# Performance work log

Measured on AMD Instinct MI355X. Metric: run time of the kernel, lower is better.

The kernel has to match this reference:

```python
import jax, jax.numpy as jnp
import numpy as np

PATCHES = [(4, 4), (2, 2)]  # (width, height) per stream chunk
SCALE = 2
DM = 256


def conv2d(x, w, bias, pad=0):
    y = jax.lax.conv_general_dilated(
        x, w, window_strides=(1, 1), padding=[(pad, pad), (pad, pad)],
        dimension_numbers=("NCHW", "OIHW", "NCHW"))
    return y + bias[None, :, None, None]


def to_patches(x, b, t, dk, out_h, ph, out_w, pw):
    # x: [b*t, dk, out_h*ph, out_w*pw] -> [b, t*out_h*out_w, dk*ph*pw]
    x = x.reshape(b, t, dk, out_h, ph, out_w, pw)
    return x.transpose(0, 1, 3, 5, 2, 4, 6).reshape(b, t * out_h * out_w, dk * ph * pw)


def from_patches(y, b, t, dk, out_h, ph, out_w, pw):
    # y: [b, t*out_h*out_w, dk*ph*pw] -> [b*t, dk, out_h*ph, out_w*pw]
    y = y.reshape(b, t, out_h, out_w, dk, ph, pw)
    return y.transpose(0, 1, 4, 2, 5, 3, 6).reshape(b * t, dk, out_h * ph, out_w * pw)


def attention(q, k, v):
    d = q.shape[-1]
    scores = jnp.einsum("bnd,bmd->bnm", q, k) / jnp.sqrt(jnp.asarray(d, q.dtype))
    p = jax.nn.softmax(scores, axis=-1)
    return jnp.einsum("bnm,bmd->bnd", p, v)


def forward(x_lo, x_hi, b,
            wq_lo, bq_lo, wk_lo, bk_lo, wv_lo, bv_lo,
            wq_hi, bq_hi, wk_hi, bk_hi, wv_hi, bv_hi,
            wo_lo, bo_lo, wo_hi, bo_hi):
    bt_lo, _, h, w = x_lo.shape
    bt_hi, _, h_, w_ = x_hi.shape
    t_lo = bt_lo // b
    t_hi = bt_hi // b
    n_p = len(PATCHES)
    d_k_lo = DM * SCALE ** 2 // n_p
    d_k_hi = DM // n_p

    q_lo_all = conv2d(x_lo, wq_lo, bq_lo)
    k_lo_all = conv2d(x_lo, wk_lo, bk_lo)
    v_lo_all = conv2d(x_lo, wv_lo, bv_lo)
    q_hi_all = conv2d(x_hi, wq_hi, bq_hi)
    k_hi_all = conv2d(x_hi, wk_hi, bk_hi)
    v_hi_all = conv2d(x_hi, wv_hi, bv_hi)

    outs_lo, outs_hi = [], []
    for i, (width, height) in enumerate(PATCHES):
        out_w, out_h = w // width, h // height
        sl_lo = slice(i * d_k_lo, (i + 1) * d_k_lo)
        sl_hi = slice(i * d_k_hi, (i + 1) * d_k_hi)
        ql = to_patches(q_lo_all[:, sl_lo], b, t_lo, d_k_lo, out_h, height, out_w, width)
        kl = to_patches(k_lo_all[:, sl_lo], b, t_lo, d_k_lo, out_h, height, out_w, width)
        vl = to_patches(v_lo_all[:, sl_lo], b, t_lo, d_k_lo, out_h, height, out_w, width)
        qh = to_patches(q_hi_all[:, sl_hi], b, t_hi, d_k_hi, out_h, height * SCALE, out_w, width * SCALE)
        kh = to_patches(k_hi_all[:, sl_hi], b, t_hi, d_k_hi, out_h, height * SCALE, out_w, width * SCALE)
        vh = to_patches(v_hi_all[:, sl_hi], b, t_hi, d_k_hi, out_h, height * SCALE, out_w, width * SCALE)

        q = jnp.concatenate([ql, qh], axis=1)
        k = jnp.concatenate([kl, kh], axis=1)
        v = jnp.concatenate([vl, vh], axis=1)
        y = attention(q, k, v)

        n_lo = t_lo * out_h * out_w
        y_lo = from_patches(y[:, :n_lo], b, t_lo, d_k_lo, out_h, height, out_w, width)
        y_hi = from_patches(y[:, n_lo:], b, t_hi, d_k_hi, out_h, height * SCALE, out_w, width * SCALE)
        outs_lo.append(y_lo)
        outs_hi.append(y_hi)

    out_lo = jnp.concatenate(outs_lo, axis=1)
    out_hi = jnp.concatenate(outs_hi, axis=1)
    out_lo = jax.nn.leaky_relu(conv2d(out_lo, wo_lo, bo_lo, pad=1), 0.2)
    out_hi = jax.nn.leaky_relu(conv2d(out_hi, wo_hi, bo_hi, pad=1), 0.2)
    return out_lo, out_hi


def setup_inputs() -> dict:
    key = jax.random.key(0)
    ks = jax.random.split(key, 12)
    dm2 = DM * SCALE ** 2  # 1024
    s = 0.02
    inp = {
        "x_lo": jax.random.normal(ks[0], (16, DM, 32, 32), jnp.float32),
        "x_hi": jax.random.normal(ks[1], (16, DM, 64, 64), jnp.float32),
        "b": 4,
        "wq_lo": jax.random.normal(ks[2], (dm2, DM, 1, 1), jnp.float32) * s,
        "bq_lo": jnp.zeros((dm2,), jnp.float32),
        "wk_lo": jax.random.normal(ks[3], (dm2, DM, 1, 1), jnp.float32) * s,
        "bk_lo": jnp.zeros((dm2,), jnp.float32),
        "wv_lo": jax.random.normal(ks[4], (dm2, DM, 1, 1), jnp.float32) * s,
        "bv_lo": jnp.zeros((dm2,), jnp.float32),
        "wq_hi": jax.random.normal(ks[5], (DM, DM, 1, 1), jnp.float32) * s,
        "bq_hi": jnp.zeros((DM,), jnp.float32),
        "wk_hi": jax.random.normal(ks[6], (DM, DM, 1, 1), jnp.float32) * s,
        "bk_hi": jnp.zeros((DM,), jnp.float32),
        "wv_hi": jax.random.normal(ks[7], (DM, DM, 1, 1), jnp.float32) * s,
        "bv_hi": jnp.zeros((DM,), jnp.float32),
        "wo_lo": jax.random.normal(ks[8], (DM, dm2, 3, 3), jnp.float32) * s,
        "bo_lo": jnp.zeros((DM,), jnp.float32),
        "wo_hi": jax.random.normal(ks[9], (DM, DM, 3, 3), jnp.float32) * s,
        "bo_hi": jnp.zeros((DM,), jnp.float32),
    }
    return inp


def reference(x_lo, x_hi, b,
              wq_lo, bq_lo, wk_lo, bk_lo, wv_lo, bv_lo,
              wq_hi, bq_hi, wk_hi, bk_hi, wv_hi, bv_hi,
              wo_lo, bo_lo, wo_hi, bo_hi):
    return forward(x_lo, x_hi, b,
                   wq_lo, bq_lo, wk_lo, bk_lo, wv_lo, bv_lo,
                   wq_hi, bq_hi, wk_hi, bk_hi, wv_hi, bv_hi,
                   wo_lo, bo_lo, wo_hi, bo_hi)
```

## Files before the change

kernel.cpp:

```cpp
#include <hip/hip_runtime.h>
#include <hip/hip_bf16.h>
#include <stdint.h>

typedef __attribute__((ext_vector_type(8))) short short8;
typedef __attribute__((ext_vector_type(4))) short short4v;
typedef __attribute__((ext_vector_type(2))) short short2v;
typedef __attribute__((ext_vector_type(4))) float floatx4;

__device__ __forceinline__ unsigned short f2b(float f) {
  unsigned u = __builtin_bit_cast(unsigned, f);
  unsigned r = u + 0x7fffu + ((u >> 16) & 1u);
  return (unsigned short)(r >> 16);
}
__device__ __forceinline__ float b2f(unsigned short h) {
  unsigned u = ((unsigned)h) << 16;
  return __builtin_bit_cast(float, u);
}
__device__ __forceinline__ void glds16(const unsigned short* src, unsigned short* dst) {
  __builtin_amdgcn_global_load_lds((const __attribute__((address_space(1))) void*)src,
                                   (__attribute__((address_space(3))) void*)dst, 16, 0, 0);
}
__device__ __forceinline__ int swz(int r, int o) {
  return (r << 9) + (o ^ ((((o >> 7) & 3) ^ (r & 7)) << 4));
}
__device__ __forceinline__ void xcd_remap(int& bx, int& by, int& bz) {
  const int gx = gridDim.x, gy = gridDim.y;
  const int nwg = gx * gy * (int)gridDim.z;
  int lin = bx + gx * (by + gy * bz);
  lin = (lin & 7) * (nwg >> 3) + (lin >> 3);
  bx = lin % gx; const int r = lin / gx;
  by = r % gy; bz = r / gy;
}

struct GemmP {
  const unsigned short* A;
  const unsigned short* B;
  long sAb, sBb;
  int lda, ldb, K;
  unsigned short* C; long sCb; int ldc;
  const float* bias;
  unsigned short *Q0, *K0, *V0t, *Q1, *K1, *V1t;
};

template<int EPI>
__global__ __launch_bounds__(512) void gemm256(GemmP p) {
  __shared__ __align__(16) unsigned short LDS[65536];
  const int tid = threadIdx.x;
  const int wv = tid >> 6, lane = tid & 63;
  const int wm = wv >> 2, wn = wv & 3;
  const int g = lane >> 4, l16 = lane & 15;
  int bx = blockIdx.x, by = blockIdx.y, bz = blockIdx.z;
  xcd_remap(bx, by, bz);
  const int m0 = by * 256, n0 = bx * 256;

  int bb = bz, koff = 0, Keff = p.K;
  if constexpr (EPI == 1) { bb = bz >> 4; koff = (bz & 15) * (p.K >> 4); Keff = p.K >> 4; }
  const unsigned short* Ab = p.A + (long)bb * p.sAb + (long)m0 * p.lda + koff;
  const unsigned short* Bb = p.B + (long)bb * p.sBb + (long)n0 * p.ldb + koff;
  const int NT = Keff >> 5;

  const int r0 = tid >> 2;
  const int cs = (tid & 3) ^ ((r0 >> 1) & 3);
  const unsigned short* aS0 = Ab + (long)r0 * p.lda + cs * 8;
  const unsigned short* aS1 = aS0 + (long)128 * p.lda;
  const unsigned short* bS0 = Bb + (long)r0 * p.ldb + cs * 8;
  const unsigned short* bS1 = bS0 + (long)128 * p.ldb;
  unsigned short* const lds0 = (unsigned short*)LDS;
  const int wbase = wv * 512;

  auto STAGE_A = [&](int t) {
    unsigned short* d = lds0 + (t & 3) * 16384;
    const long ko = (long)t * 32;
    glds16(aS0 + ko, d + wbase);
    glds16(aS1 + ko, d + 4096 + wbase);
  };
  auto STAGE_B = [&](int t) {
    unsigned short* d = lds0 + (t & 3) * 16384 + 8192;
    const long ko = (long)t * 32;
    glds16(bS0 + ko, d + wbase);
    glds16(bS1 + ko, d + 4096 + wbase);
  };

  STAGE_A(0); STAGE_B(0); STAGE_A(1); STAGE_B(1); STAGE_A(2); STAGE_B(2);

  floatx4 acc[8][4];
  const floatx4 z4 = {0.f, 0.f, 0.f, 0.f};
#pragma unroll
  for (int i = 0; i < 8; ++i)
#pragma unroll
    for (int j = 0; j < 4; ++j) acc[i][j] = z4;

  const int loff = l16 * 32 + ((g ^ ((l16 >> 1) & 3)) * 8);
  const int aRowB = wm * 128;

  asm volatile("s_waitcnt vmcnt(8)" ::: "memory");
  __builtin_amdgcn_s_barrier();
  short8 bf[4], af[4];
#pragma unroll
  for (int ni = 0; ni < 4; ++ni)
    bf[ni] = *(const short8*)(lds0 + 8192 + (wn * 64 + ni * 16) * 32 + loff);
#pragma unroll
  for (int mi = 0; mi < 4; ++mi)
    af[mi] = *(const short8*)(lds0 + (aRowB + mi * 16) * 32 + loff);

  for (int t = 0; t < NT; ++t) {
    const unsigned short* As = lds0 + (t & 3) * 16384;
    const unsigned short* AsN = lds0 + ((t + 1) & 3) * 16384;
    if (t < NT - 2) asm volatile("s_waitcnt vmcnt(4)" ::: "memory");
    else            asm volatile("s_waitcnt vmcnt(0)" ::: "memory");
    __builtin_amdgcn_s_barrier();
    __builtin_amdgcn_sched_barrier(0);
    if (t + 3 < NT) STAGE_A(t + 3);
    short8 ag[4];
#pragma unroll
    for (int mi = 0; mi < 4; ++mi)
      ag[mi] = *(const short8*)(As + (aRowB + 64 + mi * 16) * 32 + loff);
    __builtin_amdgcn_s_setprio(1);
#pragma unroll
    for (int mi = 0; mi < 4; ++mi)
#pragma unroll
      for (int ni = 0; ni < 4; ++ni)
        acc[mi][ni] = __builtin_amdgcn_mfma_f32_16x16x32_bf16(af[mi], bf[ni], acc[mi][ni], 0, 0, 0);
    __builtin_amdgcn_s_setprio(0);
    if (t + 3 < NT) STAGE_B(t + 3);
    short8 bfN[4], afN[4];
    if (t + 1 < NT) {
      const unsigned short* BsN = AsN + 8192;
#pragma unroll
      for (int ni = 0; ni < 4; ++ni)
        bfN[ni] = *(const short8*)(BsN + (wn * 64 + ni * 16) * 32 + loff);
#pragma unroll
      for (int mi = 0; mi < 4; ++mi)
        afN[mi] = *(const short8*)(AsN + (aRowB + mi * 16) * 32 + loff);
    }
    __builtin_amdgcn_s_setprio(1);
#pragma unroll
    for (int mi = 0; mi < 4; ++mi)
#pragma unroll
      for (int ni = 0; ni < 4; ++ni)
        acc[4 + mi][ni] = __builtin_amdgcn_mfma_f32_16x16x32_bf16(ag[mi], bf[ni], acc[4 + mi][ni], 0, 0, 0);
    __builtin_amdgcn_s_setprio(0);
    if (t + 1 < NT) {
#pragma unroll
      for (int i = 0; i < 4; ++i) { bf[i] = bfN[i]; af[i] = afN[i]; }
    }
  }

  if constexpr (EPI == 1) {
    unsigned short* C = p.C + (long)bz * p.sCb;
#pragma unroll
    for (int mi = 0; mi < 8; ++mi) {
#pragma unroll
      for (int ni = 0; ni < 4; ++ni) {
        const int col = n0 + wn * 64 + ni * 16 + l16;
#pragma unroll
        for (int r4 = 0; r4 < 4; ++r4) {
          const int row = m0 + wm * 128 + mi * 16 + g * 4 + r4;
          C[(long)row * p.ldc + col] = f2b(acc[mi][ni][r4]);
        }
      }
    }
  } else {
    __syncthreads();
    char* shb = (char*)LDS;
    const int sel = (EPI == 2) ? (m0 >> 10) : (m0 >> 8);
#pragma unroll
    for (int mi = 0; mi < 8; ++mi) {
#pragma unroll
      for (int ni = 0; ni < 4; ++ni) {
        const int c = wn * 64 + ni * 16 + l16;
#pragma unroll
        for (int r4 = 0; r4 < 4; ++r4) {
          const int rr = wm * 128 + mi * 16 + g * 4 + r4;
          float v = acc[mi][ni][r4];
          if constexpr (EPI == 2 || EPI == 3) {
            v += p.bias[m0 + rr];
            if (sel == 0) {
              float sc;
              if constexpr (EPI == 2) sc = ((m0 & 1023) < 512) ? 0.011048543456039806f
                                                               : 0.02209708691207961f;
              else                    sc = (rr < 128) ? 0.011048543456039806f
                                                      : 0.02209708691207961f;
              v *= sc;
            }
          }
          *(unsigned short*)(shb + swz(rr, c * 2)) = f2b(v);
        }
      }
    }
    __syncthreads();

    if constexpr (EPI == 0) {
      unsigned short* C = p.C + (long)bz * p.sCb;
#pragma unroll
      for (int j = 0; j < 16; ++j) {
        const int e = j * 512 + tid;
        const int r = e >> 5, ck = e & 31;
        short8 v = *(const short8*)(shb + swz(r, ck * 16));
        *(short8*)(C + (long)(m0 + r) * p.ldc + n0 + ck * 8) = v;
      }
    } else if constexpr (EPI == 2) {
      const int chb = m0 & 1023;
      const bool cfg0 = chb < 512;
      const int b = bz >> 2, tt = bz & 3;
      const int k0 = n0 >> 8;
      unsigned short* dst = cfg0 ? (sel == 0 ? p.Q0 : sel == 1 ? p.K0 : p.V0t)
                                 : (sel == 0 ? p.Q1 : sel == 1 ? p.K1 : p.V1t);
      if (sel != 2) {
        if (cfg0) {
          const long base = (long)(b * 512) * 8192;
#pragma unroll
          for (int j = 0; j < 16; ++j) {
            const int e = j * 512 + tid;
            const int pi = e >> 9, idx2 = e & 511;
            const int ch = idx2 >> 1, hf = idx2 & 1;
            const int oyL = pi >> 3, ox = pi & 7;
            const int nseq = (tt * 8 + 2 * k0 + oyL) * 8 + ox;
            const int yl = oyL * 4 + hf * 2;
            short4v a = *(const short4v*)(shb + swz(ch, (yl * 32 + ox * 4) * 2));
            short4v b2 = *(const short4v*)(shb + swz(ch, ((yl + 1) * 32 + ox * 4) * 2));
            short8 v = {a[0], a[1], a[2], a[3], b2[0], b2[1], b2[2], b2[3]};
            *(short8*)(dst + base + (long)nseq * 8192 + (chb + ch) * 16 + hf * 8) = v;
          }
        } else {
          const int c2lo = chb - 512;
          const long base = (long)(b * 2048) * 2048;
#pragma unroll
          for (int j = 0; j < 16; ++j) {
            const int e = j * 512 + tid;
            const int pi = e >> 7, cp = e & 127;
            const int oyL = pi >> 4, ox = pi & 15;
            const int nseq = (tt * 16 + 4 * k0 + oyL) * 16 + ox;
            short8 v;
#pragma unroll
            for (int rr = 0; rr < 2; ++rr) {
#pragma unroll
              for (int k = 0; k < 2; ++k) {
                short2v pr = *(const short2v*)(shb +
                    swz(cp * 2 + rr, ((oyL * 2 + k) * 32 + ox * 2) * 2));
                v[rr * 4 + k * 2] = pr[0];
                v[rr * 4 + k * 2 + 1] = pr[1];
              }
            }
            *(short8*)(dst + base + (long)nseq * 2048 + (c2lo + cp * 2) * 4) = v;
          }
        }
      } else {
        if (cfg0) {
          const long base = (long)(b * 8192) * 512;
#pragma unroll
          for (int j = 0; j < 16; ++j) {
            const int e = j * 512 + tid;
            const int oyL = e >> 12, fu = e & 4095;
            const int ch = fu >> 4, pp = fu & 15;
            const int py = pp >> 2, px = pp & 3;
            const int yl = oyL * 4 + py;
            short8 v;
#pragma unroll
            for (int ox = 0; ox < 8; ++ox)
              v[ox] = *(const unsigned short*)(shb + swz(ch, (yl * 32 + ox * 4 + px) * 2));
            const long f = (long)(chb + ch) * 16 + pp;
            *(short8*)(dst + base + f * 512 + (tt * 8 + 2 * k0 + oyL) * 8) = v;
          }
        } else {
          const int c2lo = chb - 512;
          const long base = (long)(b * 2048) * 2048;
#pragma unroll
          for (int j = 0; j < 16; ++j) {
            const int e = j * 512 + tid;
            const int he = e & 1, oyL = (e >> 1) & 3, fu = e >> 3;
            const int c2 = fu >> 2, pp = fu & 3;
            const int py = pp >> 1, px = pp & 1;
            const int yl = oyL * 2 + py;
            short8 v;
#pragma unroll
            for (int i = 0; i < 8; ++i) {
              const int ox = he * 8 + i;
              v[i] = *(const unsigned short*)(shb + swz(c2, (yl * 32 + ox * 2 + px) * 2));
            }
            const long f = (long)(c2lo + c2) * 4 + pp;
            *(short8*)(dst + base + f * 2048 + (tt * 16 + 4 * k0 + oyL) * 16 + he * 8) = v;
          }
        }
      }
    } else if constexpr (EPI == 3) {
      const int b = bz >> 2, tt = bz & 3;
      const int k0 = n0 >> 8;
      const int oyA = k0 >> 1, pyb = (k0 & 1) * 4;
      unsigned short* dstA = sel == 0 ? p.Q0 : sel == 1 ? p.K0 : p.V0t;
      unsigned short* dstB = sel == 0 ? p.Q1 : sel == 1 ? p.K1 : p.V1t;
      if (sel != 2) {
#pragma unroll
        for (int j = 0; j < 16; ++j) {
          const int e = j * 512 + tid;
          if (e < 4096) {
            const int ox = e >> 9, cy = e & 511;
            const int ch = cy >> 2, yl = cy & 3;
            const int nseq = 256 + (tt * 8 + oyA) * 8 + ox;
            short8 v = *(const short8*)(shb + swz(ch, (yl * 64 + ox * 8) * 2));
            *(short8*)(dstA + ((long)(b * 512 + nseq)) * 8192 + ch * 64 + (pyb + yl) * 8) = v;
          } else {
            const int ee = e - 4096;
            const int ox = ee >> 8, cc = ee & 255;
            const int c2 = cc >> 1, hf = cc & 1;
            const int nseq = 1024 + (tt * 16 + k0) * 16 + ox;
            short8 v;
#pragma unroll
            for (int k = 0; k < 2; ++k) {
              short4v a = *(const short4v*)(shb +
                  swz(128 + c2, ((hf * 2 + k) * 64 + ox * 4) * 2));
              v[k * 4] = a[0]; v[k * 4 + 1] = a[1]; v[k * 4 + 2] = a[2]; v[k * 4 + 3] = a[3];
            }
            *(short8*)(dstB + ((long)(b * 2048 + nseq)) * 2048 + c2 * 16 + hf * 8) = v;
          }
        }
      } else {
#pragma unroll
        for (int j = 0; j < 16; ++j) {
          const int e = j * 512 + tid;
          if (e < 4096) {
            const int ch = e >> 5, yl = (e >> 3) & 3, px = e & 7;
            short8 v;
#pragma unroll
            for (int ox = 0; ox < 8; ++ox)
              v[ox] = *(const unsigned short*)(shb + swz(ch, (yl * 64 + ox * 8 + px) * 2));
            const long f = (long)ch * 64 + (pyb + yl) * 8 + px;
            *(short8*)(dstA + ((long)b * 8192 + f) * 512 + 256 + (tt * 8 + oyA) * 8) = v;
          } else {
            const int ee = e - 4096;
            const int he = ee & 1, fu = ee >> 1;
            const int c2 = fu >> 4, pp = fu & 15;
            const int py = pp >> 2, px = pp & 3;
            short8 v;
#pragma unroll
            for (int i = 0; i < 8; ++i) {
              const int x = (he * 8 + i) * 4 + px;
              v[i] = *(const unsigned short*)(shb + swz(128 + c2, (py * 64 + x) * 2));
            }
            const long f = (long)c2 * 16 + pp;
            *(short8*)(dstB + ((long)b * 2048 + f) * 2048 + 1024 + (tt * 16 + k0) * 16 + he * 8) = v;
          }
        }
      }
    } else if constexpr (EPI == 4) {
      const int b = bz;
      if (m0 == 0) {
        const int chbase = n0 >> 4;
        unsigned short* dst = p.Q0;
#pragma unroll
        for (int j = 0; j < 16; ++j) {
          const int e = j * 512 + tid;
          const int hf = e & 1, pp = (e >> 1) & 15, rr = e >> 5;
          const int t = rr >> 6, oh = (rr >> 3) & 7, ow = rr & 7;
          const int bt = b * 4 + t;
          const int py = pp >> 2, px = pp & 3;
          short8 v;
#pragma unroll
          for (int i = 0; i < 8; ++i)
            v[i] = *(const unsigned short*)(shb + swz(rr, ((hf * 8 + i) * 16 + pp) * 2));
          *(short8*)(dst + (((long)bt * 34 + oh * 4 + py + 1) * 34 + ow * 4 + px + 1) * 1024
                     + chbase + hf * 8) = v;
        }
      } else {
        const int chbase = n0 >> 6;
        unsigned short* dst = p.Q1;
#pragma unroll
        for (int j = 0; j < 32; ++j) {
          const int e = j * 512 + tid;
          const int pp = e & 63, rr = e >> 6;
          const int t = rr >> 6, oh = (rr >> 3) & 7, ow = rr & 7;
          const int bt = b * 4 + t;
          const int py = pp >> 3, px = pp & 7;
          short4v v;
#pragma unroll
          for (int i = 0; i < 4; ++i)
            v[i] = *(const unsigned short*)(shb + swz(rr, (i * 64 + pp) * 2));
          *(short4v*)(dst + (((long)bt * 66 + oh * 8 + py + 1) * 66 + ow * 8 + px + 1) * 256
                      + chbase) = v;
        }
      }
    } else if constexpr (EPI == 5) {
      const int b = bz;
      if (m0 < 1024) {
        const int chbase = n0 >> 2;
        unsigned short* dst = p.Q0;
#pragma unroll
        for (int j = 0; j < 16; ++j) {
          const int e = j * 512 + tid;
          const int ch8 = e & 7, pp = (e >> 3) & 3, rr = e >> 5;
          const int n = m0 + rr;
          const int t = n >> 8, oh = (n >> 4) & 15, ow = n & 15;
          const int bt = b * 4 + t;
          const int py = pp >> 1, px = pp & 1;
          short8 v;
#pragma unroll
          for (int i = 0; i < 8; ++i)
            v[i] = *(const unsigned short*)(shb + swz(rr, ((ch8 * 8 + i) * 4 + pp) * 2));
          *(short8*)(dst + (((long)bt * 34 + oh * 2 + py + 1) * 34 + ow * 2 + px + 1) * 1024
                     + 512 + chbase + ch8 * 8) = v;
        }
      } else {
        const int chbase = n0 >> 4;
        unsigned short* dst = p.Q1;
#pragma unroll
        for (int j = 0; j < 16; ++j) {
          const int e = j * 512 + tid;
          const int hf = e & 1, pp = (e >> 1) & 15, rr = e >> 5;
          const int m = m0 + rr - 1024;
          const int t = m >> 8, oh = (m >> 4) & 15, ow = m & 15;
          const int bt = b * 4 + t;
          const int py = pp >> 2, px = pp & 3;
          short8 v;
#pragma unroll
          for (int i = 0; i < 8; ++i)
            v[i] = *(const unsigned short*)(shb + swz(rr, ((hf * 8 + i) * 16 + pp) * 2));
          *(short8*)(dst + (((long)bt * 66 + oh * 4 + py + 1) * 66 + ow * 4 + px + 1) * 256
                     + 128 + chbase + hf * 8) = v;
        }
      }
    }
  }
}

template<int H, int W, int CIN, int KS, bool PARTIAL>
__global__ __launch_bounds__(512) void conv256(const unsigned short* __restrict__ Cinp,
                                               const unsigned short* __restrict__ Wt,
                                               const float* __restrict__ bias,
                                               float* __restrict__ out,
                                               unsigned short* __restrict__ P0,
                                               unsigned short* __restrict__ P1) {
  constexpr int HP = H + 2, WP = W + 2;
  constexpr int CC = CIN / KS;
  constexpr int NT = 9 * CC / 32;
  __shared__ __align__(16) unsigned short LDS[65536];
  const int tid = threadIdx.x;
  const int wv = tid >> 6, lane = tid & 63;
  const int wm = wv >> 2, wn = wv & 3;
  const int g = lane >> 4, l16 = lane & 15;
  int bx = blockIdx.x, by = blockIdx.y, bz = blockIdx.z;
  xcd_remap(bx, by, bz);
  const int bt = bz / KS, ks = bz % KS;
  const int n0 = bx * 256;

  const int r0 = tid >> 2;
  const int cs = (tid & 3) ^ ((r0 >> 1) & 3);
  const unsigned short* wA0 = Wt + (long)r0 * CIN + ks * CC + cs * 8;
  const unsigned short* wA1 = wA0 + (long)128 * CIN;
  const int p0 = n0 + r0, p1 = p0 + 128;
  const int y0p = p0 / W, x0p = p0 % W;
  const int y1p = p1 / W, x1p = p1 % W;
  const unsigned short* cB = Cinp + (long)bt * HP * WP * CIN + ks * CC + cs * 8;
  const unsigned short* pB0 = cB + ((long)y0p * WP + x0p) * CIN;
  const unsigned short* pB1 = cB + ((long)y1p * WP + x1p) * CIN;
  unsigned short* const lds0 = (unsigned short*)LDS;
  const int wbase = wv * 512;

  auto STAGE_A = [&](int t) {
    unsigned short* d = lds0 + (t & 3) * 16384;
    const int tap = t >> 3, tc = (t & 7) * 32;
    const long off = (long)tap * (256L * CIN) + tc;
    glds16(wA0 + off, d + wbase);
    glds16(wA1 + off, d + 4096 + wbase);
  };
  auto STAGE_B = [&](int t) {
    unsigned short* d = lds0 + (t & 3) * 16384 + 8192;
    const int tap = t >> 3, tc = (t & 7) * 32;
    const int ky = tap / 3, kx = tap - ky * 3;
    const long off = ((long)ky * WP + kx) * CIN + tc;
    glds16(pB0 + off, d + wbase);
    glds16(pB1 + off, d + 4096 + wbase);
  };

  STAGE_A(0); STAGE_B(0); STAGE_A(1); STAGE_B(1); STAGE_A(2); STAGE_B(2);

  floatx4 acc[8][4];
  const floatx4 z4 = {0.f, 0.f, 0.f, 0.f};
#pragma unroll
  for (int i = 0; i < 8; ++i)
#pragma unroll
    for (int j = 0; j < 4; ++j) acc[i][j] = z4;

  const int loff = l16 * 32 + ((g ^ ((l16 >> 1) & 3)) * 8);
  const int aRowB = wm * 128;

  asm volatile("s_waitcnt vmcnt(8)" ::: "memory");
  __builtin_amdgcn_s_barrier();
  short8 bf[4], af[4];
#pragma unroll
  for (int ni = 0; ni < 4; ++ni)
    bf[ni] = *(const short8*)(lds0 + 8192 + (wn * 64 + ni * 16) * 32 + loff);
#pragma unroll
  for (int mi = 0; mi < 4; ++mi)
    af[mi] = *(const short8*)(lds0 + (aRowB + mi * 16) * 32 + loff);

  for (int t = 0; t < NT; ++t) {
    const unsigned short* As = lds0 + (t & 3) * 16384;
    const unsigned short* AsN = lds0 + ((t + 1) & 3) * 16384;
    if (t < NT - 2) asm volatile("s_waitcnt vmcnt(4)" ::: "memory");
    else            asm volatile("s_waitcnt vmcnt(0)" ::: "memory");
    __builtin_amdgcn_s_barrier();
    __builtin_amdgcn_sched_barrier(0);
    if (t + 3 < NT) STAGE_A(t + 3);
    short8 ag[4];
#pragma unroll
    for (int mi = 0; mi < 4; ++mi)
      ag[mi] = *(const short8*)(As + (aRowB + 64 + mi * 16) * 32 + loff);
    __builtin_amdgcn_s_setprio(1);
#pragma unroll
    for (int mi = 0; mi < 4; ++mi)
#pragma unroll
      for (int ni = 0; ni < 4; ++ni)
        acc[mi][ni] = __builtin_amdgcn_mfma_f32_16x16x32_bf16(af[mi], bf[ni], acc[mi][ni], 0, 0, 0);
    __builtin_amdgcn_s_setprio(0);
    if (t + 3 < NT) STAGE_B(t + 3);
    short8 bfN[4], afN[4];
    if (t + 1 < NT) {
      const unsigned short* BsN = AsN + 8192;
#pragma unroll
      for (int ni = 0; ni < 4; ++ni)
        bfN[ni] = *(const short8*)(BsN + (wn * 64 + ni * 16) * 32 + loff);
#pragma unroll
      for (int mi = 0; mi < 4; ++mi)
        afN[mi] = *(const short8*)(AsN + (aRowB + mi * 16) * 32 + loff);
    }
    __builtin_amdgcn_s_setprio(1);
#pragma unroll
    for (int mi = 0; mi < 4; ++mi)
#pragma unroll
      for (int ni = 0; ni < 4; ++ni)
        acc[4 + mi][ni] = __builtin_amdgcn_mfma_f32_16x16x32_bf16(ag[mi], bf[ni], acc[4 + mi][ni], 0, 0, 0);
    __builtin_amdgcn_s_setprio(0);
    if (t + 1 < NT) {
#pragma unroll
      for (int i = 0; i < 4; ++i) { bf[i] = bfN[i]; af[i] = afN[i]; }
    }
  }

  if constexpr (!PARTIAL) {
#pragma unroll
    for (int mi = 0; mi < 8; ++mi) {
#pragma unroll
      for (int ni = 0; ni < 4; ++ni) {
        const int pn = n0 + wn * 64 + ni * 16 + l16;
        const int y = pn / W, x = pn % W;
#pragma unroll
        for (int r4 = 0; r4 < 4; ++r4) {
          const int co = wm * 128 + mi * 16 + g * 4 + r4;
          float v = acc[mi][ni][r4] + bias[co];
          v = v > 0.f ? v : 0.2f * v;
          out[(((long)bt * 256 + co) * H + y) * W + x] = v;
        }
      }
    }
  } else {
    unsigned short* pout = (ks < 2 ? P0 : P1) + (long)(ks & 1) * (16L * 256 * H * W);
#pragma unroll
    for (int mi = 0; mi < 8; ++mi) {
#pragma unroll
      for (int ni = 0; ni < 4; ++ni) {
        const int pn = n0 + wn * 64 + ni * 16 + l16;
        const int y = pn / W, x = pn % W;
#pragma unroll
        for (int r4 = 0; r4 < 4; ++r4) {
          const int co = wm * 128 + mi * 16 + g * 4 + r4;
          pout[(((long)bt * 256 + co) * H + y) * W + x] = f2b(acc[mi][ni][r4]);
        }
      }
    }
  }
}

template<int L>
__global__ __launch_bounds__(256) void softmax_rows(unsigned short* S) {
  const int w = threadIdx.x >> 6, lane = threadIdx.x & 63;
  const long row = (long)blockIdx.x * 4 + w;
  unsigned short* R = S + row * L;
  constexpr int NC = L / 64;
  float v[NC];
  float m = -1e30f;
#pragma unroll
  for (int i = 0; i < NC; ++i) { v[i] = b2f(R[i * 64 + lane]); m = fmaxf(m, v[i]); }
#pragma unroll
  for (int off = 32; off; off >>= 1) m = fmaxf(m, __shfl_xor(m, off, 64));
  float s = 0.f;
#pragma unroll
  for (int i = 0; i < NC; ++i) { v[i] = __expf(v[i] - m); s += v[i]; }
#pragma unroll
  for (int off = 32; off; off >>= 1) s += __shfl_xor(s, off, 64);
  const float inv = 1.0f / s;
#pragma unroll
  for (int i = 0; i < NC; ++i) R[i * 64 + lane] = f2b(v[i] * inv);
}

__global__ __launch_bounds__(256) void softmax_red16(const unsigned short* __restrict__ P,
                                                     unsigned short* __restrict__ S) {
  const int w = threadIdx.x >> 6, lane = threadIdx.x & 63;
  const int rowg = blockIdx.x * 4 + w;
  const int b = rowg >> 9, n = rowg & 511;
  const unsigned short* base = P + ((long)b * 16) * 262144 + (long)n * 512 + lane;
  float v[8];
#pragma unroll
  for (int i = 0; i < 8; ++i) {
    float s = 0.f;
#pragma unroll
    for (int ks = 0; ks < 16; ++ks) s += b2f(base[(long)ks * 262144 + i * 64]);
    v[i] = s;
  }
  float m = -1e30f;
#pragma unroll
  for (int i = 0; i < 8; ++i) m = fmaxf(m, v[i]);
#pragma unroll
  for (int off = 32; off; off >>= 1) m = fmaxf(m, __shfl_xor(m, off, 64));
  float s = 0.f;
#pragma unroll
  for (int i = 0; i < 8; ++i) { v[i] = __expf(v[i] - m); s += v[i]; }
#pragma unroll
  for (int off = 32; off; off >>= 1) s += __shfl_xor(s, off, 64);
  const float inv = 1.0f / s;
  unsigned short* R = S + (long)rowg * 512;
#pragma unroll
  for (int i = 0; i < 8; ++i) R[i * 64 + lane] = f2b(v[i] * inv);
}

__global__ __launch_bounds__(256) void xt_both(const float* __restrict__ x_lo,
                                               unsigned short* __restrict__ xt_lo,
                                               const float* __restrict__ x_hi,
                                               unsigned short* __restrict__ xt_hi) {
  __shared__ unsigned short tile[64 * 65];
  const int tid = threadIdx.x;
  const int blk = blockIdx.x;
  const float* x; unsigned short* xt; int NPIX, bxx, byy, bzz;
  if (blk < 1024) {
    x = x_lo; xt = xt_lo; NPIX = 1024;
    bxx = blk & 15; byy = (blk >> 4) & 3; bzz = blk >> 6;
  } else {
    const int q = blk - 1024;
    x = x_hi; xt = xt_hi; NPIX = 4096;
    bxx = q & 63; byy = (q >> 6) & 3; bzz = q >> 8;
  }
  const int ch0 = byy * 64;
  const long pix0 = (long)bxx * 64;
  const float* src = x + ((long)bzz * 256 + ch0) * NPIX + pix0;
#pragma unroll
  for (int i = 0; i < 16; ++i) {
    const int lin = i * 256 + tid;
    const int ch = lin >> 6, px = lin & 63;
    tile[ch * 65 + px] = f2b(src[(long)ch * NPIX + px]);
  }
  __syncthreads();
  unsigned short* dst = xt + ((long)bzz * NPIX + pix0) * 256 + ch0;
#pragma unroll
  for (int i = 0; i < 16; ++i) {
    const int lin = i * 256 + tid;
    const int px = lin >> 6, ch = lin & 63;
    dst[(long)px * 256 + ch] = tile[ch * 65 + px];
  }
}

__global__ void prep_qkv_both(const float* wq_lo, const float* wk_lo, const float* wv_lo,
                              const float* bq_lo, const float* bk_lo, const float* bv_lo,
                              unsigned short* Wcat_lo, float* Bcat_lo,
                              const float* wq_hi, const float* wk_hi, const float* wv_hi,
                              const float* bq_hi, const float* bk_hi, const float* bv_hi,
                              unsigned short* Wcat_hi, float* Bcat_hi) {
  const int blk = blockIdx.x;
  const float *wq, *wk, *wv, *bq, *bk, *bv;
  unsigned short* Wcat; float* Bcat; int CO, idx;
  if (blk < 3072) {
    wq = wq_lo; wk = wk_lo; wv = wv_lo; bq = bq_lo; bk = bk_lo; bv = bv_lo;
    Wcat = Wcat_lo; Bcat = Bcat_lo; CO = 1024;
    idx = blk * 256 + threadIdx.x;
  } else {
    wq = wq_hi; wk = wk_hi; wv = wv_hi; bq = bq_hi; bk = bk_hi; bv = bv_hi;
    Wcat = Wcat_hi; Bcat = Bcat_hi; CO = 256;
    idx = (blk - 3072) * 256 + threadIdx.x;
  }
  const int n = 3 * CO * 256;
  if (idx < n) {
    const int sel = idx / (CO * 256);
    const int r = idx - sel * CO * 256;
    const float* wsel = sel == 0 ? wq : (sel == 1 ? wk : wv);
    Wcat[idx] = f2b(wsel[r]);
  }
  if (idx < 3 * CO) {
    const int sel = idx / CO;
    const int r = idx - sel * CO;
    const float* bsel = sel == 0 ? bq : (sel == 1 ? bk : bv);
    Bcat[idx] = bsel[r];
  }
}

__global__ __launch_bounds__(256) void prep_conv_both(const float* __restrict__ wo_lo,
                                                      unsigned short* __restrict__ Wt_lo,
                                                      const float* __restrict__ wo_hi,
                                                      unsigned short* __restrict__ Wt_hi) {
  __shared__ unsigned short T[9216];
  const int blk = blockIdx.x;
  const int tid = threadIdx.x;
  if (blk < 256) {
    const int o0 = blk;
    const float* src = wo_lo + (long)o0 * 1024 * 9;
    for (int j = tid; j < 9216; j += 256) {
      const int t9 = j % 9, r = j / 9;
      T[t9 * 1024 + r] = f2b(src[j]);
    }
    __syncthreads();
#pragma unroll
    for (int t9 = 0; t9 < 9; ++t9)
      for (int j = tid; j < 1024; j += 256)
        Wt_lo[((long)t9 * 256 + o0) * 1024 + j] = T[t9 * 1024 + j];
  } else {
    const int o0 = (blk - 256) * 4;
    const float* src = wo_hi + (long)o0 * 256 * 9;
    for (int j = tid; j < 9216; j += 256) {
      const int t9 = j % 9, r = j / 9;
      T[t9 * 1024 + r] = f2b(src[j]);
    }
    __syncthreads();
#pragma unroll
    for (int t9 = 0; t9 < 9; ++t9)
      for (int j = tid; j < 1024; j += 256) {
        const int oo = j >> 8, i = j & 255;
        Wt_hi[((long)t9 * 256 + o0 + oo) * 256 + i] = T[t9 * 1024 + j];
      }
  }
}

__global__ __launch_bounds__(256) void zero_both(unsigned short* lo, unsigned short* hi) {
  const int blk = blockIdx.x;
  unsigned short* buf; int HP, WP, C; long i;
  if (blk < 1056) { buf = lo; HP = 34; WP = 34; C = 1024; i = (long)blk * 256 + threadIdx.x; }
  else            { buf = hi; HP = 66; WP = 66; C = 256;  i = (long)(blk - 1056) * 256 + threadIdx.x; }
  const int per_px = C >> 3;
  const int strip = 2 * WP + 2 * (HP - 2);
  const long tot = (long)16 * strip * per_px;
  if (i >= tot) return;
  const int c8 = (int)(i % per_px);
  const long r = i / per_px;
  const int s = (int)(r % strip);
  const int bt = (int)(r / strip);
  int y, x;
  if (s < WP) { y = 0; x = s; }
  else if (s < 2 * WP) { y = HP - 1; x = s - WP; }
  else if (s < 2 * WP + (HP - 2)) { y = s - 2 * WP + 1; x = 0; }
  else { y = s - 2 * WP - (HP - 2) + 1; x = WP - 1; }
  const short8 z = {0, 0, 0, 0, 0, 0, 0, 0};
  *(short8*)(buf + (((long)bt * HP + y) * WP + x) * C + c8 * 8) = z;
}

__global__ __launch_bounds__(256) void reduce_lrelu(const unsigned short* __restrict__ P0,
                                                    const unsigned short* __restrict__ P1,
                                                    const float* __restrict__ bias,
                                                    float* __restrict__ out) {
  const long i = (long)blockIdx.x * 256 + threadIdx.x;
  const long flat = i * 8;
  constexpr long SL = 4194304;
  short8 a = *(const short8*)(P0 + flat);
  short8 b = *(const short8*)(P0 + SL + flat);
  short8 c = *(const short8*)(P1 + flat);
  short8 d = *(const short8*)(P1 + SL + flat);
  const int co = ((int)(flat >> 10)) & 255;
  const float bv = bias[co];
  floatx4 r0, r1;
#pragma unroll
  for (int j = 0; j < 8; ++j) {
    float v = b2f((unsigned short)a[j]) + b2f((unsigned short)b[j]) +
              b2f((unsigned short)c[j]) + b2f((unsigned short)d[j]) + bv;
    v = v > 0.f ? v : 0.2f * v;
    if (j < 4) r0[j] = v; else r1[j - 4] = v;
  }
  *(floatx4*)(out + flat) = r0;
  *(floatx4*)(out + flat + 4) = r1;
}

extern "C" void kernel_launch(void* const* d_in, const int* in_sizes, int n_in,
                              void* d_out, int out_size, void* d_ws, size_t ws_size,
                              hipStream_t stream) {
  (void)in_sizes; (void)n_in; (void)out_size; (void)ws_size;
  const float* x_lo = (const float*)d_in[0];
  const float* x_hi = (const float*)d_in[1];
  const float* wq_lo = (const float*)d_in[3];
  const float* bq_lo = (const float*)d_in[4];
  const float* wk_lo = (const float*)d_in[5];
  const float* bk_lo = (const float*)d_in[6];
  const float* wv_lo = (const float*)d_in[7];
  const float* bv_lo = (const float*)d_in[8];
  const float* wq_hi = (const float*)d_in[9];
  const float* bq_hi = (const float*)d_in[10];
  const float* wk_hi = (const float*)d_in[11];
  const float* bk_hi = (const float*)d_in[12];
  const float* wv_hi = (const float*)d_in[13];
  const float* bv_hi = (const float*)d_in[14];
  const float* wo_lo = (const float*)d_in[15];
  const float* bo_lo = (const float*)d_in[16];
  const float* wo_hi = (const float*)d_in[17];
  const float* bo_hi = (const float*)d_in[18];
  float* out = (float*)d_out;

  char* ws = (char*)d_ws;
  const long B0 = 33554432;
  unsigned short* Qp0 = (unsigned short*)(ws);
  unsigned short* Kp0 = (unsigned short*)(ws + B0);
  unsigned short* V0t = (unsigned short*)(ws + 2 * B0);
  unsigned short* Qp1 = (unsigned short*)(ws + 3 * B0);
  unsigned short* Kp1 = (unsigned short*)(ws + 4 * B0);
  unsigned short* V1t = (unsigned short*)(ws + 5 * B0);
  char* ptr = ws + 6 * B0;
  unsigned short* S0 = (unsigned short*)ptr;     ptr += 2097152;
  unsigned short* Xt_lo = (unsigned short*)ptr;  ptr += 8388608;
  unsigned short* Xt_hi = (unsigned short*)ptr;  ptr += 33554432;
  unsigned short* Wcat_lo = (unsigned short*)ptr; ptr += 1572864;
  unsigned short* Wcat_hi = (unsigned short*)ptr; ptr += 393216;
  float* Bcat_lo = (float*)ptr;                  ptr += 12288;
  float* Bcat_hi = (float*)ptr;                  ptr += 3072;
  unsigned short* Wt_lo = (unsigned short*)ptr;  ptr += 4718592;
  unsigned short* Wt_hi = (unsigned short*)ptr;  ptr += 1179648;
  unsigned short* S0p = Xt_hi;
  unsigned short* S1 = Xt_hi;
  unsigned short* CinP_lo = Qp0;
  unsigned short* CinP_hi = Qp1;
  unsigned short* PC0 = V0t;
  unsigned short* PC1 = V1t;

  prep_qkv_both<<<3840, 256, 0, stream>>>(
      wq_lo, wk_lo, wv_lo, bq_lo, bk_lo, bv_lo, Wcat_lo, Bcat_lo,
      wq_hi, wk_hi, wv_hi, bq_hi, bk_hi, bv_hi, Wcat_hi, Bcat_hi);
  prep_conv_both<<<320, 256, 0, stream>>>(wo_lo, Wt_lo, wo_hi, Wt_hi);
  xt_both<<<5120, 256, 0, stream>>>(x_lo, Xt_lo, x_hi, Xt_hi);

  {
    GemmP p{};
    p.A = Wcat_lo; p.B = Xt_lo; p.sAb = 0; p.sBb = 1024L * 256;
    p.lda = 256; p.ldb = 256; p.K = 256;
    p.bias = Bcat_lo;
    p.Q0 = Qp0; p.K0 = Kp0; p.V0t = V0t; p.Q1 = Qp1; p.K1 = Kp1; p.V1t = V1t;
    gemm256<2><<<dim3(4, 12, 16), 512, 0, stream>>>(p);
    p.A = Wcat_hi; p.B = Xt_hi; p.sBb = 4096L * 256; p.bias = Bcat_hi;
    gemm256<3><<<dim3(16, 3, 16), 512, 0, stream>>>(p);
  }

  {
    GemmP s{};
    s.A = Qp0; s.B = Kp0; s.sAb = 512L * 8192; s.sBb = 512L * 8192;
    s.lda = 8192; s.ldb = 8192; s.K = 8192;
    s.C = S0p; s.sCb = 262144; s.ldc = 512;
    gemm256<1><<<dim3(2, 2, 64), 512, 0, stream>>>(s);
    softmax_red16<<<512, 256, 0, stream>>>(S0p, S0);
  }

  {
    GemmP s{};
    s.A = Qp1; s.B = Kp1; s.sAb = 2048L * 2048; s.sBb = 2048L * 2048;
    s.lda = 2048; s.ldb = 2048; s.K = 2048;
    s.C = S1; s.sCb = 2048L * 2048; s.ldc = 2048;
    gemm256<0><<<dim3(8, 8, 4), 512, 0, stream>>>(s);
    softmax_rows<2048><<<2048, 256, 0, stream>>>(S1);
  }

  zero_both<<<1576, 256, 0, stream>>>(CinP_lo, CinP_hi);
  {
    GemmP pv{};
    pv.A = S0; pv.B = V0t; pv.sAb = 512L * 512; pv.sBb = 8192L * 512;
    pv.lda = 512; pv.ldb = 512; pv.K = 512;
    pv.Q0 = CinP_lo; pv.Q1 = CinP_hi;
    gemm256<4><<<dim3(32, 2, 4), 512, 0, stream>>>(pv);
  }
  {
    GemmP pv{};
    pv.A = S1; pv.B = V1t; pv.sAb = 2048L * 2048; pv.sBb = 2048L * 2048;
    pv.lda = 2048; pv.ldb = 2048; pv.K = 2048;
    pv.Q0 = CinP_lo; pv.Q1 = CinP_hi;
    gemm256<5><<<dim3(8, 8, 4), 512, 0, stream>>>(pv);
  }

  conv256<32, 32, 1024, 4, true><<<dim3(4, 1, 64), 512, 0, stream>>>(
      CinP_lo, Wt_lo, bo_lo, out, PC0, PC1);
  reduce_lrelu<<<2048, 256, 0, stream>>>(PC0, PC1, bo_lo, out);
  conv256<64, 64, 256, 1, false><<<dim3(16, 1, 16), 512, 0, stream>>>(
      CinP_hi, Wt_hi, bo_hi, out + 4194304, nullptr, nullptr);
}
```

Before: 537.3 us.

## Switch GEMM and conv mainloops to BK=64 double-buffered pipeline

Both the batched GEMM and the implicit-GEMM conv kernels move from a 4-stage ring of K=32 tiles to a 2-stage double buffer of K=64 tiles. This halves the number of barriers per K and uses an 8-way XOR swizzle matched to 64-element rows. LDS fragments are now loaded inside each iteration instead of being prefetched across iterations. The trade-off is less prefetch depth: each step waits for vmcnt(0), so there is only one tile of lookahead and global-load latency may be exposed.

```diff
diff --git a/kernel.cpp b/kernel.cpp
--- a/kernel.cpp
+++ b/kernel.cpp
@@ -57,31 +57,30 @@
   if constexpr (EPI == 1) { bb = bz >> 4; koff = (bz & 15) * (p.K >> 4); Keff = p.K >> 4; }
   const unsigned short* Ab = p.A + (long)bb * p.sAb + (long)m0 * p.lda + koff;
   const unsigned short* Bb = p.B + (long)bb * p.sBb + (long)n0 * p.ldb + koff;
-  const int NT = Keff >> 5;
-
-  const int r0 = tid >> 2;
-  const int cs = (tid & 3) ^ ((r0 >> 1) & 3);
-  const unsigned short* aS0 = Ab + (long)r0 * p.lda + cs * 8;
-  const unsigned short* aS1 = aS0 + (long)128 * p.lda;
-  const unsigned short* bS0 = Bb + (long)r0 * p.ldb + cs * 8;
-  const unsigned short* bS1 = bS0 + (long)128 * p.ldb;
+  const int NT = Keff >> 6;
+
+  const int r0 = tid >> 3;
+  const int cs8 = (tid & 7) ^ (r0 & 7);
+  const unsigned short* aS[4];
+  const unsigned short* bS[4];
+#pragma unroll
+  for (int i = 0; i < 4; ++i) {
+    aS[i] = Ab + (long)(r0 + 64 * i) * p.lda + cs8 * 8;
+    bS[i] = Bb + (long)(r0 + 64 * i) * p.ldb + cs8 * 8;
+  }
   unsigned short* const lds0 = (unsigned short*)LDS;
   const int wbase = wv * 512;
 
-  auto STAGE_A = [&](int t) {
-    unsigned short* d = lds0 + (t & 3) * 16384;
-    const long ko = (long)t * 32;
-    glds16(aS0 + ko, d + wbase);
-    glds16(aS1 + ko, d + 4096 + wbase);
+  auto STAGE = [&](int t) {
+    unsigned short* d = lds0 + (t & 1) * 32768;
+    const long ko = (long)t * 64;
+#pragma unroll
+    for (int i = 0; i < 4; ++i) glds16(aS[i] + ko, d + i * 4096 + wbase);
+#pragma unroll
+    for (int i = 0; i < 4; ++i) glds16(bS[i] + ko, d + 16384 + i * 4096 + wbase);
   };
-  auto STAGE_B = [&](int t) {
-    unsigned short* d = lds0 + (t & 3) * 16384 + 8192;
-    const long ko = (long)t * 32;
-    glds16(bS0 + ko, d + wbase);
-    glds16(bS1 + ko, d + 4096 + wbase);
-  };
-
-  STAGE_A(0); STAGE_B(0); STAGE_A(1); STAGE_B(1); STAGE_A(2); STAGE_B(2);
+
+  STAGE(0);
 
   floatx4 acc[8][4];
   const floatx4 z4 = {0.f, 0.f, 0.f, 0.f};
@@ -90,59 +89,42 @@
 #pragma unroll
     for (int j = 0; j < 4; ++j) acc[i][j] = z4;
 
-  const int loff = l16 * 32 + ((g ^ ((l16 >> 1) & 3)) * 8);
+  const int lmask = l16 & 7;
+  const int loff0 = l16 * 64 + ((g ^ lmask) * 8);
   const int aRowB = wm * 128;
 
-  asm volatile("s_waitcnt vmcnt(8)" ::: "memory");
-  __builtin_amdgcn_s_barrier();
-  short8 bf[4], af[4];
-#pragma unroll
-  for (int ni = 0; ni < 4; ++ni)
-    bf[ni] = *(const short8*)(lds0 + 8192 + (wn * 64 + ni * 16) * 32 + loff);
-#pragma unroll
-  for (int mi = 0; mi < 4; ++mi)
-    af[mi] = *(const short8*)(lds0 + (aRowB + mi * 16) * 32 + loff);
-
   for (int t = 0; t < NT; ++t) {
-    const unsigned short* As = lds0 + (t & 3) * 16384;
-    const unsigned short* AsN = lds0 + ((t + 1) & 3) * 16384;
-    if (t < NT - 2) asm volatile("s_waitcnt vmcnt(4)" ::: "memory");
-    else            asm volatile("s_waitcnt vmcnt(0)" ::: "memory");
+    const unsigned short* As = lds0 + (t & 1) * 32768;
+    const unsigned short* Bs = As + 16384;
+    asm volatile("s_waitcnt vmcnt(0)" ::: "memory");
     __builtin_amdgcn_s_barrier();
     __builtin_amdgcn_sched_barrier(0);
-    if (t + 3 < NT) STAGE_A(t + 3);
-    short8 ag[4];
-#pragma unroll
-    for (int mi = 0; mi < 4; ++mi)
-      ag[mi] = *(const short8*)(As + (aRowB + 64 + mi * 16) * 32 + loff);
-    __builtin_amdgcn_s_setprio(1);
-#pragma unroll
-    for (int mi = 0; mi < 4; ++mi)
+    if (t + 1 < NT) STAGE(t + 1);
+#pragma unroll
+    for (int kk = 0; kk < 2; ++kk) {
+      const int lo = loff0 ^ (kk * 32);
+      short8 bf[4], af[4], ag[4];
 #pragma unroll
       for (int ni = 0; ni < 4; ++ni)
-        acc[mi][ni] = __builtin_amdgcn_mfma_f32_16x16x32_bf16(af[mi], bf[ni], acc[mi][ni], 0, 0, 0);
-    __builtin_amdgcn_s_setprio(0);
-    if (t + 3 < NT) STAGE_B(t + 3);
-    short8 bfN[4], afN[4];
-    if (t + 1 < NT) {
-      const unsigned short* BsN = AsN + 8192;
-#pragma unroll
-      for (int ni = 0; ni < 4; ++ni)
-        bfN[ni] = *(const short8*)(BsN + (wn * 64 + ni * 16) * 32 + loff);
+        bf[ni] = *(const short8*)(Bs + (wn * 64 + ni * 16) * 64 + lo);
 #pragma unroll
       for (int mi = 0; mi < 4; ++mi)
-        afN[mi] = *(const short8*)(AsN + (aRowB + mi * 16) * 32 + loff);
-    }
-    __builtin_amdgcn_s_setprio(1);
-#pragma unroll
-    for (int mi = 0; mi < 4; ++mi)
-#pragma unroll
-      for (int ni = 0; ni < 4; ++ni)
-        acc[4 + mi][ni] = __builtin_amdgcn_mfma_f32_16x16x32_bf16(ag[mi], bf[ni], acc[4 + mi][ni], 0, 0, 0);
-    __builtin_amdgcn_s_setprio(0);
-    if (t + 1 < NT) {
-#pragma unroll
-      for (int i = 0; i < 4; ++i) { bf[i] = bfN[i]; af[i] = afN[i]; }
+        af[mi] = *(const short8*)(As + (aRowB + mi * 16) * 64 + lo);
+#pragma unroll
+      for (int mi = 0; mi < 4; ++mi)
+        ag[mi] = *(const short8*)(As + (aRowB + 64 + mi * 16) * 64 + lo);
+      __builtin_amdgcn_s_setprio(1);
+#pragma unroll
+      for (int mi = 0; mi < 4; ++mi)
+#pragma unroll
+        for (int ni = 0; ni < 4; ++ni)
+          acc[mi][ni] = __builtin_amdgcn_mfma_f32_16x16x32_bf16(af[mi], bf[ni], acc[mi][ni], 0, 0, 0);
+#pragma unroll
+      for (int mi = 0; mi < 4; ++mi)
+#pragma unroll
+        for (int ni = 0; ni < 4; ++ni)
+          acc[4 + mi][ni] = __builtin_amdgcn_mfma_f32_16x16x32_bf16(ag[mi], bf[ni], acc[4 + mi][ni], 0, 0, 0);
+      __builtin_amdgcn_s_setprio(0);
     }
   }
 
@@ -431,7 +413,7 @@
                                                unsigned short* __restrict__ P1) {
   constexpr int HP = H + 2, WP = W + 2;
   constexpr int CC = CIN / KS;
-  constexpr int NT = 9 * CC / 32;
+  constexpr int NT = 9 * CC / 64;
   __shared__ __align__(16) unsigned short LDS[65536];
   const int tid = threadIdx.x;
   const int wv = tid >> 6, lane = tid & 63;
@@ -442,36 +424,35 @@
   const int bt = bz / KS, ks = bz % KS;
   const int n0 = bx * 256;
 
-  const int r0 = tid >> 2;
-  const int cs = (tid & 3) ^ ((r0 >> 1) & 3);
-  const unsigned short* wA0 = Wt + (long)r0 * CIN + ks * CC + cs * 8;
-  const unsigned short* wA1 = wA0 + (long)128 * CIN;
-  const int p0 = n0 + r0, p1 = p0 + 128;
-  const int y0p = p0 / W, x0p = p0 % W;
-  const int y1p = p1 / W, x1p = p1 % W;
-  const unsigned short* cB = Cinp + (long)bt * HP * WP * CIN + ks * CC + cs * 8;
-  const unsigned short* pB0 = cB + ((long)y0p * WP + x0p) * CIN;
-  const unsigned short* pB1 = cB + ((long)y1p * WP + x1p) * CIN;
+  const int r0 = tid >> 3;
+  const int cs8 = (tid & 7) ^ (r0 & 7);
+  const unsigned short* wA[4];
+  const unsigned short* pB[4];
+#pragma unroll
+  for (int i = 0; i < 4; ++i)
+    wA[i] = Wt + (long)(r0 + 64 * i) * CIN + ks * CC + cs8 * 8;
+  const unsigned short* cB = Cinp + (long)bt * HP * WP * CIN + ks * CC + cs8 * 8;
+#pragma unroll
+  for (int i = 0; i < 4; ++i) {
+    const int pp = n0 + r0 + 64 * i;
+    pB[i] = cB + ((long)(pp / W) * WP + (pp % W)) * CIN;
+  }
   unsigned short* const lds0 = (unsigned short*)LDS;
   const int wbase = wv * 512;
 
-  auto STAGE_A = [&](int t) {
-    unsigned short* d = lds0 + (t & 3) * 16384;
-    const int tap = t >> 3, tc = (t & 7) * 32;
-    const long off = (long)tap * (256L * CIN) + tc;
-    glds16(wA0 + off, d + wbase);
-    glds16(wA1 + off, d + 4096 + wbase);
+  auto STAGE = [&](int t) {
+    unsigned short* d = lds0 + (t & 1) * 32768;
+    const int tap = t >> 2, tc = (t & 3) * 64;
+    const long offA = (long)tap * (256L * CIN) + tc;
+    const int ky = tap / 3, kx = tap - ky * 3;
+    const long offB = ((long)ky * WP + kx) * CIN + tc;
+#pragma unroll
+    for (int i = 0; i < 4; ++i) glds16(wA[i] + offA, d + i * 4096 + wbase);
+#pragma unroll
+    for (int i = 0; i < 4; ++i) glds16(pB[i] + offB, d + 16384 + i * 4096 + wbase);
   };
-  auto STAGE_B = [&](int t) {
-    unsigned short* d = lds0 + (t & 3) * 16384 + 8192;
-    const int tap = t >> 3, tc = (t & 7) * 32;
-    const int ky = tap / 3, kx = tap - ky * 3;
-    const long off = ((long)ky * WP + kx) * CIN + tc;
-    glds16(pB0 + off, d + wbase);
-    glds16(pB1 + off, d + 4096 + wbase);
-  };
-
-  STAGE_A(0); STAGE_B(0); STAGE_A(1); STAGE_B(1); STAGE_A(2); STAGE_B(2);
+
+  STAGE(0);
 
   floatx4 acc[8][4];
   const floatx4 z4 = {0.f, 0.f, 0.f, 0.f};
@@ -480,59 +461,42 @@
 #pragma unroll
     for (int j = 0; j < 4; ++j) acc[i][j] = z4;
 
-  const int loff = l16 * 32 + ((g ^ ((l16 >> 1) & 3)) * 8);
+  const int lmask = l16 & 7;
+  const int loff0 = l16 * 64 + ((g ^ lmask) * 8);
   const int aRowB = wm * 128;
 
-  asm volatile("s_waitcnt vmcnt(8)" ::: "memory");
-  __builtin_amdgcn_s_barrier();
-  short8 bf[4], af[4];
-#pragma unroll
-  for (int ni = 0; ni < 4; ++ni)
-    bf[ni] = *(const short8*)(lds0 + 8192 + (wn * 64 + ni * 16) * 32 + loff);
-#pragma unroll
-  for (int mi = 0; mi < 4; ++mi)
-    af[mi] = *(const short8*)(lds0 + (aRowB + mi * 16) * 32 + loff);
-
   for (int t = 0; t < NT; ++t) {
-    const unsigned short* As = lds0 + (t & 3) * 16384;
-    const unsigned short* AsN = lds0 + ((t + 1) & 3) * 16384;
-    if (t < NT - 2) asm volatile("s_waitcnt vmcnt(4)" ::: "memory");
-    else            asm volatile("s_waitcnt vmcnt(0)" ::: "memory");
+    const unsigned short* As = lds0 + (t & 1) * 32768;
+    const unsigned short* Bs = As + 16384;
+    asm volatile("s_waitcnt vmcnt(0)" ::: "memory");
     __builtin_amdgcn_s_barrier();
     __builtin_amdgcn_sched_barrier(0);
-    if (t + 3 < NT) STAGE_A(t + 3);
-    short8 ag[4];
-#pragma unroll
-    for (int mi = 0; mi < 4; ++mi)
-      ag[mi] = *(const short8*)(As + (aRowB + 64 + mi * 16) * 32 + loff);
-    __builtin_amdgcn_s_setprio(1);
-#pragma unroll
-    for (int mi = 0; mi < 4; ++mi)
+    if (t + 1 < NT) STAGE(t + 1);
+#pragma unroll
+    for (int kk = 0; kk < 2; ++kk) {
+      const int lo = loff0 ^ (kk * 32);
+      short8 bf[4], af[4], ag[4];
 #pragma unroll
       for (int ni = 0; ni < 4; ++ni)
-        acc[mi][ni] = __builtin_amdgcn_mfma_f32_16x16x32_bf16(af[mi], bf[ni], acc[mi][ni], 0, 0, 0);
-    __builtin_amdgcn_s_setprio(0);
-    if (t + 3 < NT) STAGE_B(t + 3);
-    short8 bfN[4], afN[4];
-    if (t + 1 < NT) {
-      const unsigned short* BsN = AsN + 8192;
-#pragma unroll
-      for (int ni = 0; ni < 4; ++ni)
-        bfN[ni] = *(const short8*)(BsN + (wn * 64 + ni * 16) * 32 + loff);
+        bf[ni] = *(const short8*)(Bs + (wn * 64 + ni * 16) * 64 + lo);
 #pragma unroll
       for (int mi = 0; mi < 4; ++mi)
-        afN[mi] = *(const short8*)(AsN + (aRowB + mi * 16) * 32 + loff);
-    }
-    __builtin_amdgcn_s_setprio(1);
-#pragma unroll
-    for (int mi = 0; mi < 4; ++mi)
-#pragma unroll
-      for (int ni = 0; ni < 4; ++ni)
-        acc[4 + mi][ni] = __builtin_amdgcn_mfma_f32_16x16x32_bf16(ag[mi], bf[ni], acc[4 + mi][ni], 0, 0, 0);
-    __builtin_amdgcn_s_setprio(0);
-    if (t + 1 < NT) {
-#pragma unroll
-      for (int i = 0; i < 4; ++i) { bf[i] = bfN[i]; af[i] = afN[i]; }
+        af[mi] = *(const short8*)(As + (aRowB + mi * 16) * 64 + lo);
+#pragma unroll
+      for (int mi = 0; mi < 4; ++mi)
+        ag[mi] = *(const short8*)(As + (aRowB + 64 + mi * 16) * 64 + lo);
+      __builtin_amdgcn_s_setprio(1);
+#pragma unroll
+      for (int mi = 0; mi < 4; ++mi)
+#pragma unroll
+        for (int ni = 0; ni < 4; ++ni)
+          acc[mi][ni] = __builtin_amdgcn_mfma_f32_16x16x32_bf16(af[mi], bf[ni], acc[mi][ni], 0, 0, 0);
+#pragma unroll
+      for (int mi = 0; mi < 4; ++mi)
+#pragma unroll
+        for (int ni = 0; ni < 4; ++ni)
+          acc[4 + mi][ni] = __builtin_amdgcn_mfma_f32_16x16x32_bf16(ag[mi], bf[ni], acc[4 + mi][ni], 0, 0, 0);
+      __builtin_amdgcn_s_setprio(0);
     }
   }
 
```

New measurement: 512.8 us, median of 2. -4.6%, faster.

## Switch gemm256 to BK=64 double-buffered LDS pipeline with wider swizzle

Applied to the files above, without the earlier changes.

The GEMM main loop now stages K-tiles of 64 instead of 32, using two LDS buffers instead of a four-deep ring of 32-wide tiles. Each iteration issues the next whole tile's global-to-LDS loads, waits for all outstanding loads, and runs two 32-wide MFMA sub-steps. The LDS swizzle is reworked for 64-element rows. This halves the number of barriers and loop iterations, but shortens prefetch depth to one tile and drops the register double-buffering of fragments, so memory latency may be less hidden.

```diff
diff --git a/kernel.cpp b/kernel.cpp
--- a/kernel.cpp
+++ b/kernel.cpp
@@ -57,31 +57,30 @@
   if constexpr (EPI == 1) { bb = bz >> 4; koff = (bz & 15) * (p.K >> 4); Keff = p.K >> 4; }
   const unsigned short* Ab = p.A + (long)bb * p.sAb + (long)m0 * p.lda + koff;
   const unsigned short* Bb = p.B + (long)bb * p.sBb + (long)n0 * p.ldb + koff;
-  const int NT = Keff >> 5;
-
-  const int r0 = tid >> 2;
-  const int cs = (tid & 3) ^ ((r0 >> 1) & 3);
-  const unsigned short* aS0 = Ab + (long)r0 * p.lda + cs * 8;
-  const unsigned short* aS1 = aS0 + (long)128 * p.lda;
-  const unsigned short* bS0 = Bb + (long)r0 * p.ldb + cs * 8;
-  const unsigned short* bS1 = bS0 + (long)128 * p.ldb;
+  const int NT = Keff >> 6;
+
+  const int r0 = tid >> 3;
+  const int cs8 = (tid & 7) ^ (r0 & 7);
+  const unsigned short* aS[4];
+  const unsigned short* bS[4];
+#pragma unroll
+  for (int i = 0; i < 4; ++i) {
+    aS[i] = Ab + (long)(r0 + 64 * i) * p.lda + cs8 * 8;
+    bS[i] = Bb + (long)(r0 + 64 * i) * p.ldb + cs8 * 8;
+  }
   unsigned short* const lds0 = (unsigned short*)LDS;
   const int wbase = wv * 512;
 
-  auto STAGE_A = [&](int t) {
-    unsigned short* d = lds0 + (t & 3) * 16384;
-    const long ko = (long)t * 32;
-    glds16(aS0 + ko, d + wbase);
-    glds16(aS1 + ko, d + 4096 + wbase);
+  auto STAGE = [&](int t) {
+    unsigned short* d = lds0 + (t & 1) * 32768;
+    const long ko = (long)t * 64;
+#pragma unroll
+    for (int i = 0; i < 4; ++i) glds16(aS[i] + ko, d + i * 4096 + wbase);
+#pragma unroll
+    for (int i = 0; i < 4; ++i) glds16(bS[i] + ko, d + 16384 + i * 4096 + wbase);
   };
-  auto STAGE_B = [&](int t) {
-    unsigned short* d = lds0 + (t & 3) * 16384 + 8192;
-    const long ko = (long)t * 32;
-    glds16(bS0 + ko, d + wbase);
-    glds16(bS1 + ko, d + 4096 + wbase);
-  };
-
-  STAGE_A(0); STAGE_B(0); STAGE_A(1); STAGE_B(1); STAGE_A(2); STAGE_B(2);
+
+  STAGE(0);
 
   floatx4 acc[8][4];
   const floatx4 z4 = {0.f, 0.f, 0.f, 0.f};
@@ -90,59 +89,42 @@
 #pragma unroll
     for (int j = 0; j < 4; ++j) acc[i][j] = z4;
 
-  const int loff = l16 * 32 + ((g ^ ((l16 >> 1) & 3)) * 8);
+  const int lmask = l16 & 7;
+  const int loff0 = l16 * 64 + ((g ^ lmask) * 8);
   const int aRowB = wm * 128;
 
-  asm volatile("s_waitcnt vmcnt(8)" ::: "memory");
-  __builtin_amdgcn_s_barrier();
-  short8 bf[4], af[4];
-#pragma unroll
-  for (int ni = 0; ni < 4; ++ni)
-    bf[ni] = *(const short8*)(lds0 + 8192 + (wn * 64 + ni * 16) * 32 + loff);
-#pragma unroll
-  for (int mi = 0; mi < 4; ++mi)
-    af[mi] = *(const short8*)(lds0 + (aRowB + mi * 16) * 32 + loff);
-
   for (int t = 0; t < NT; ++t) {
-    const unsigned short* As = lds0 + (t & 3) * 16384;
-    const unsigned short* AsN = lds0 + ((t + 1) & 3) * 16384;
-    if (t < NT - 2) asm volatile("s_waitcnt vmcnt(4)" ::: "memory");
-    else            asm volatile("s_waitcnt vmcnt(0)" ::: "memory");
+    const unsigned short* As = lds0 + (t & 1) * 32768;
+    const unsigned short* Bs = As + 16384;
+    asm volatile("s_waitcnt vmcnt(0)" ::: "memory");
     __builtin_amdgcn_s_barrier();
     __builtin_amdgcn_sched_barrier(0);
-    if (t + 3 < NT) STAGE_A(t + 3);
-    short8 ag[4];
-#pragma unroll
-    for (int mi = 0; mi < 4; ++mi)
-      ag[mi] = *(const short8*)(As + (aRowB + 64 + mi * 16) * 32 + loff);
-    __builtin_amdgcn_s_setprio(1);
-#pragma unroll
-    for (int mi = 0; mi < 4; ++mi)
+    if (t + 1 < NT) STAGE(t + 1);
+#pragma unroll
+    for (int kk = 0; kk < 2; ++kk) {
+      const int lo = loff0 ^ (kk * 32);
+      short8 bf[4], af[4], ag[4];
 #pragma unroll
       for (int ni = 0; ni < 4; ++ni)
-        acc[mi][ni] = __builtin_amdgcn_mfma_f32_16x16x32_bf16(af[mi], bf[ni], acc[mi][ni], 0, 0, 0);
-    __builtin_amdgcn_s_setprio(0);
-    if (t + 3 < NT) STAGE_B(t + 3);
-    short8 bfN[4], afN[4];
-    if (t + 1 < NT) {
-      const unsigned short* BsN = AsN + 8192;
-#pragma unroll
-      for (int ni = 0; ni < 4; ++ni)
-        bfN[ni] = *(const short8*)(BsN + (wn * 64 + ni * 16) * 32 + loff);
+        bf[ni] = *(const short8*)(Bs + (wn * 64 + ni * 16) * 64 + lo);
 #pragma unroll
       for (int mi = 0; mi < 4; ++mi)
-        afN[mi] = *(const short8*)(AsN + (aRowB + mi * 16) * 32 + loff);
-    }
-    __builtin_amdgcn_s_setprio(1);
-#pragma unroll
-    for (int mi = 0; mi < 4; ++mi)
-#pragma unroll
-      for (int ni = 0; ni < 4; ++ni)
-        acc[4 + mi][ni] = __builtin_amdgcn_mfma_f32_16x16x32_bf16(ag[mi], bf[ni], acc[4 + mi][ni], 0, 0, 0);
-    __builtin_amdgcn_s_setprio(0);
-    if (t + 1 < NT) {
-#pragma unroll
-      for (int i = 0; i < 4; ++i) { bf[i] = bfN[i]; af[i] = afN[i]; }
+        af[mi] = *(const short8*)(As + (aRowB + mi * 16) * 64 + lo);
+#pragma unroll
+      for (int mi = 0; mi < 4; ++mi)
+        ag[mi] = *(const short8*)(As + (aRowB + 64 + mi * 16) * 64 + lo);
+      __builtin_amdgcn_s_setprio(1);
+#pragma unroll
+      for (int mi = 0; mi < 4; ++mi)
+#pragma unroll
+        for (int ni = 0; ni < 4; ++ni)
+          acc[mi][ni] = __builtin_amdgcn_mfma_f32_16x16x32_bf16(af[mi], bf[ni], acc[mi][ni], 0, 0, 0);
+#pragma unroll
+      for (int mi = 0; mi < 4; ++mi)
+#pragma unroll
+        for (int ni = 0; ni < 4; ++ni)
+          acc[4 + mi][ni] = __builtin_amdgcn_mfma_f32_16x16x32_bf16(ag[mi], bf[ni], acc[4 + mi][ni], 0, 0, 0);
+      __builtin_amdgcn_s_setprio(0);
     }
   }
 
```

After: 516.6 us. 3.8% less time.
